# Optimization experiments

Hardware: AMD Instinct MI355X
Metric: run time of the kernel (lower is better)

The kernel has to match this reference:

```python
import jax, jax.numpy as jnp
import numpy as np

N_NODES = 25000
N_EDGES = 400000
D_FEAT = 64      # 2 * per-endpoint feature dim (concat of both endpoints)
STATE_DIM = 16
OUT_DIM = 16
MAX_IT = 5
THRESHOLD = 0.01


def setup_inputs() -> dict:
    key = jax.random.key(0)
    ks = jax.random.split(key, 8)
    edge_src = jax.random.randint(ks[0], (N_EDGES,), 0, N_NODES)
    edge_dst = jax.random.randint(ks[1], (N_EDGES,), 0, N_NODES)
    edge_feat = jax.random.normal(ks[2], (N_EDGES, D_FEAT), jnp.float32)
    w = lambda k, s: jax.random.normal(k, s, jnp.float32) * 0.1
    return {
        "edge_feat": edge_feat,
        "Wst1": w(ks[3], (D_FEAT + STATE_DIM, 2 * STATE_DIM)),
        "bst1": jnp.zeros((2 * STATE_DIM,), jnp.float32),
        "Wst2": w(ks[4], (2 * STATE_DIM, STATE_DIM)),
        "bst2": jnp.zeros((STATE_DIM,), jnp.float32),
        "Wout1": w(ks[5], (STATE_DIM, 2 * STATE_DIM)),
        "bout1": jnp.zeros((2 * STATE_DIM,), jnp.float32),
        "Wout2": w(ks[6], (2 * STATE_DIM, OUT_DIM)),
        "bout2": jnp.zeros((OUT_DIM,), jnp.float32),
        "edge_src": edge_src,
        "edge_dst": edge_dst,
        "n_nodes": N_NODES,
    }


def reference(edge_feat, Wst1, bst1, Wst2, bst2, Wout1, bout1, Wout2, bout2,
              edge_src, edge_dst, n_nodes):
    s = Wst2.shape[1]
    state0 = jnp.zeros((n_nodes, s), edge_feat.dtype)

    def step(carry, _):
        state, done = carry
        gat = state[edge_dst]                                   # [E, s] gather
        x = jnp.concatenate([edge_feat, gat], axis=1)           # [E, 2d+s]
        res = jnp.tanh(jnp.tanh(x @ Wst1 + bst1) @ Wst2 + bst2)  # state MLP
        new_state = jax.ops.segment_sum(res, edge_src, num_segments=n_nodes)
        # per-node L2 change; stop (freeze) once all nodes are below threshold
        dist = jnp.sqrt(jnp.sum((new_state - state) ** 2, axis=1) + 1e-10)
        converged = jnp.all(dist <= THRESHOLD)
        state = jnp.where(done, state, new_state)
        return (state, done | converged), None

    (state, _), _ = jax.lax.scan(step, (state0, jnp.array(False)), None, length=MAX_IT)
    h = jnp.tanh(state @ Wout1 + bout1)
    out = jax.nn.softmax(h @ Wout2 + bout2, axis=-1)  # [n_nodes, out_dim]
    return out
```

## Files before the change

### kernel.cpp

```cpp
#include <hip/hip_runtime.h>
#include <cstddef>

#define D_FEAT 64
#define S_DIM 16
#define H_DIM 32
#define OUT_DIM 16
#define MAX_IT 5

typedef _Float16 half8 __attribute__((ext_vector_type(8)));

__device__ __forceinline__ float fast_tanh(float x) {
    float xc = fminf(fmaxf(x, -15.0f), 15.0f);
    float e = __expf(2.0f * xc);
    return (e - 1.0f) / (e + 1.0f);
}

__global__ __launch_bounds__(256)
void k_hist(const int* __restrict__ src, int* __restrict__ deg, int E) {
    int e = blockIdx.x * 256 + threadIdx.x;
    if (e < E) atomicAdd(&deg[src[e]], 1);
}

__global__ __launch_bounds__(1024)
void k_scan(const int* __restrict__ deg, int* __restrict__ cursor, int N) {
    __shared__ int wsum[16];
    __shared__ int carry;
    int lane = threadIdx.x & 63;
    int wid = threadIdx.x >> 6;
    if (threadIdx.x == 0) carry = 0;
    __syncthreads();
    for (int base = 0; base < N; base += 1024) {
        int i = base + (int)threadIdx.x;
        int v = (i < N) ? deg[i] : 0;
        int incl = v;
#pragma unroll
        for (int off = 1; off < 64; off <<= 1) {
            int t = __shfl_up(incl, off, 64);
            if (lane >= off) incl += t;
        }
        if (lane == 63) wsum[wid] = incl;
        __syncthreads();
        if (wid == 0) {
            int w = (lane < 16) ? wsum[lane] : 0;
            int wi = w;
#pragma unroll
            for (int off = 1; off < 16; off <<= 1) {
                int t = __shfl_up(wi, off, 64);
                if (lane >= off) wi += t;
            }
            if (lane < 16) wsum[lane] = wi - w;
        }
        __syncthreads();
        int excl = incl - v + wsum[wid] + carry;
        if (i < N) cursor[i] = excl;
        __syncthreads();
        if ((int)threadIdx.x == 1023) carry = excl + v;
        __syncthreads();
    }
}

__global__ __launch_bounds__(256)
void k_scatter(const int* __restrict__ src, const int* __restrict__ dst,
               int* __restrict__ cursor, int* __restrict__ pos,
               int* __restrict__ dstp, int* __restrict__ srcp, int E) {
    int e = blockIdx.x * 256 + threadIdx.x;
    if (e >= E) return;
    int s = src[e];
    int p = atomicAdd(&cursor[s], 1);
    pos[e] = p;
    dstp[p] = dst[e];
    srcp[p] = s;
}

__global__ __launch_bounds__(256)
void k_pre(const float* __restrict__ feat, const float* __restrict__ Wst1,
           const float* __restrict__ bst1, const int* __restrict__ pos,
           _Float16* __restrict__ pre, int E) {
    int e = blockIdx.x * 256 + threadIdx.x;
    if (e >= E) return;
    const float4* f4 = reinterpret_cast<const float4*>(feat + (size_t)e * D_FEAT);
    float4 f[16];
#pragma unroll
    for (int k4 = 0; k4 < 16; ++k4) f[k4] = f4[k4];
    int p = pos[e];

    float acc[H_DIM];
#pragma unroll
    for (int j = 0; j < H_DIM; ++j) acc[j] = bst1[j];
#pragma unroll
    for (int k4 = 0; k4 < 16; ++k4) {
        float4 v = f[k4];
        const float* w = Wst1 + k4 * 4 * H_DIM;
#pragma unroll
        for (int j = 0; j < H_DIM; ++j) acc[j] = fmaf(v.x, w[j], acc[j]);
#pragma unroll
        for (int j = 0; j < H_DIM; ++j) acc[j] = fmaf(v.y, w[H_DIM + j], acc[j]);
#pragma unroll
        for (int j = 0; j < H_DIM; ++j) acc[j] = fmaf(v.z, w[2 * H_DIM + j], acc[j]);
#pragma unroll
        for (int j = 0; j < H_DIM; ++j) acc[j] = fmaf(v.w, w[3 * H_DIM + j], acc[j]);
    }
    half8* op = reinterpret_cast<half8*>(pre + (size_t)p * H_DIM);
#pragma unroll
    for (int j8 = 0; j8 < 4; ++j8) {
        half8 v;
#pragma unroll
        for (int k = 0; k < 8; ++k) v[k] = (_Float16)acc[j8 * 8 + k];
        op[j8] = v;
    }
}

__global__ __launch_bounds__(256)
void k_edge(const _Float16* __restrict__ pre, const _Float16* __restrict__ nodeH16,
            const int* __restrict__ dstp, const int* __restrict__ srcp,
            const int* __restrict__ rowend, const float* __restrict__ Wst2,
            const float* __restrict__ bst2, float* __restrict__ new_state,
            const int* __restrict__ flags, int it, int E) {
#pragma unroll
    for (int j = 0; j < MAX_IT; ++j)
        if (j < it && flags[2 + j] == 0) return;
    __shared__ float sres[256][17];
    __shared__ int ssrc[256];
    __shared__ int segnode[256];
    __shared__ int segstart[256];
    __shared__ int segend[256];
    __shared__ int segflag[256];
    __shared__ int nseg;
    const int t = threadIdx.x;
    const int base = blockIdx.x * 256;
    const int ep = base + t;
    const bool valid = ep < E;
    if (t == 0) nseg = 0;

    int s = valid ? srcp[ep] : (int)0x80000000;
    ssrc[t] = s;

    if (valid) {
        half8 n0, n1, n2, n3;
        const bool useH = (it != 0);
        if (useH) {
            int d = dstp[ep];
            const half8* np = reinterpret_cast<const half8*>(nodeH16 + (size_t)d * H_DIM);
            n0 = np[0]; n1 = np[1]; n2 = np[2]; n3 = np[3];
        }
        const half8* pp = reinterpret_cast<const half8*>(pre + (size_t)ep * H_DIM);
        half8 p0 = pp[0], p1 = pp[1], p2 = pp[2], p3 = pp[3];
        float h[H_DIM];
        if (useH) {
#pragma unroll
            for (int k = 0; k < 8; ++k) {
                h[k]      = fast_tanh((float)p0[k] + (float)n0[k]);
                h[8 + k]  = fast_tanh((float)p1[k] + (float)n1[k]);
                h[16 + k] = fast_tanh((float)p2[k] + (float)n2[k]);
                h[24 + k] = fast_tanh((float)p3[k] + (float)n3[k]);
            }
        } else {
#pragma unroll
            for (int k = 0; k < 8; ++k) {
                h[k]      = fast_tanh((float)p0[k]);
                h[8 + k]  = fast_tanh((float)p1[k]);
                h[16 + k] = fast_tanh((float)p2[k]);
                h[24 + k] = fast_tanh((float)p3[k]);
            }
        }
        float r[S_DIM];
#pragma unroll
        for (int i = 0; i < S_DIM; ++i) r[i] = bst2[i];
#pragma unroll
        for (int j = 0; j < H_DIM; ++j) {
            const float* w = Wst2 + (size_t)j * S_DIM;
            float hj = h[j];
#pragma unroll
            for (int i = 0; i < S_DIM; ++i) r[i] = fmaf(hj, w[i], r[i]);
        }
#pragma unroll
        for (int i = 0; i < S_DIM; ++i) sres[t][i] = fast_tanh(r[i]);
    }
    __syncthreads();

    bool head = valid && ((t == 0) || (ssrc[t - 1] != s));
    if (head) {
        int slot = atomicAdd(&nseg, 1);
        int re = rowend[s];
        int en = re - base; if (en > 256) en = 256;
        bool tS = (t > 0) || (ep == 0) || (srcp[ep - 1] != s);
        bool tE = (re <= base + 256);
        segnode[slot] = s;
        segstart[slot] = t;
        segend[slot] = en;
        segflag[slot] = (tS && tE) ? 1 : 0;
    }
    __syncthreads();

    int ns = nseg;
    for (int w = t; w < ns * 16; w += 256) {
        int slot = w >> 4;
        int dim = w & 15;
        int st = segstart[slot];
        int en = segend[slot];
        int node = segnode[slot];
        float a = 0.f;
        for (int i = st; i < en; ++i) a += sres[i][dim];
        float* p = new_state + (size_t)node * S_DIM + dim;
        if (segflag[slot]) *p = a;
        else atomicAdd(p, a);
    }
}

__global__ __launch_bounds__(256)
void k_node(float* __restrict__ state, float* __restrict__ new_state,
            _Float16* __restrict__ nodeH16, const float* __restrict__ Wst1,
            int* __restrict__ flags, int it, int N) {
#pragma unroll
    for (int j = 0; j < MAX_IT; ++j)
        if (j < it && flags[2 + j] == 0) return;
    int tt = blockIdx.x * 256 + threadIdx.x;
    int n = tt >> 2;
    int q = tt & 3;
    if (n >= N) return;
    float4* nsp = reinterpret_cast<float4*>(new_state + (size_t)n * S_DIM);
    float4* sp = reinterpret_cast<float4*>(state + (size_t)n * S_DIM);
    float4 acc = nsp[q];
    float4 old = sp[q];
    float dx = acc.x - old.x, dy = acc.y - old.y, dz = acc.z - old.z, dw = acc.w - old.w;
    float d2 = dx * dx + dy * dy + dz * dz + dw * dw;
    sp[q] = acc;
    nsp[q] = make_float4(0.f, 0.f, 0.f, 0.f);
    d2 += __shfl_xor(d2, 1);
    d2 += __shfl_xor(d2, 2);
    if (q == 0 && d2 + 1e-10f > 1e-4f) flags[2 + it] = 1;

    float st[S_DIM];
    st[q * 4 + 0] = acc.x; st[q * 4 + 1] = acc.y; st[q * 4 + 2] = acc.z; st[q * 4 + 3] = acc.w;
#pragma unroll
    for (int m = 1; m < 4; ++m) {
        int qs = q ^ m;
        st[qs * 4 + 0] = __shfl_xor(acc.x, m);
        st[qs * 4 + 1] = __shfl_xor(acc.y, m);
        st[qs * 4 + 2] = __shfl_xor(acc.z, m);
        st[qs * 4 + 3] = __shfl_xor(acc.w, m);
    }
    float hh[8];
#pragma unroll
    for (int j = 0; j < 8; ++j) hh[j] = 0.f;
#pragma unroll
    for (int k = 0; k < S_DIM; ++k) {
        const float* w = Wst1 + (size_t)(D_FEAT + k) * H_DIM + q * 8;
        float sk = st[k];
#pragma unroll
        for (int j = 0; j < 8; ++j) hh[j] = fmaf(sk, w[j], hh[j]);
    }
    half8 hv;
#pragma unroll
    for (int j = 0; j < 8; ++j) hv[j] = (_Float16)hh[j];
    *reinterpret_cast<half8*>(nodeH16 + (size_t)n * H_DIM + q * 8) = hv;
}

__global__ __launch_bounds__(256)
void gnn_out(const float* __restrict__ state, const float* __restrict__ Wout1,
             const float* __restrict__ bout1, const float* __restrict__ Wout2,
             const float* __restrict__ bout2, float* __restrict__ out, int N) {
    int n = blockIdx.x * 256 + threadIdx.x;
    if (n >= N) return;
    float st[S_DIM];
    const float4* sp = reinterpret_cast<const float4*>(state + (size_t)n * S_DIM);
    float4 v0 = sp[0], v1 = sp[1], v2 = sp[2], v3 = sp[3];
    st[0] = v0.x; st[1] = v0.y; st[2] = v0.z; st[3] = v0.w;
    st[4] = v1.x; st[5] = v1.y; st[6] = v1.z; st[7] = v1.w;
    st[8] = v2.x; st[9] = v2.y; st[10] = v2.z; st[11] = v2.w;
    st[12] = v3.x; st[13] = v3.y; st[14] = v3.z; st[15] = v3.w;

    float h[H_DIM];
#pragma unroll
    for (int j = 0; j < H_DIM; ++j) {
        float acc = bout1[j];
#pragma unroll
        for (int k = 0; k < S_DIM; ++k) acc = fmaf(st[k], Wout1[(size_t)k * H_DIM + j], acc);
        h[j] = fast_tanh(acc);
    }
    float l[OUT_DIM];
#pragma unroll
    for (int i = 0; i < OUT_DIM; ++i) l[i] = bout2[i];
#pragma unroll
    for (int j = 0; j < H_DIM; ++j) {
        float hj = h[j];
#pragma unroll
        for (int i = 0; i < OUT_DIM; ++i) l[i] = fmaf(hj, Wout2[(size_t)j * OUT_DIM + i], l[i]);
    }
    float m = l[0];
#pragma unroll
    for (int i = 1; i < OUT_DIM; ++i) m = fmaxf(m, l[i]);
    float sum = 0.0f;
#pragma unroll
    for (int i = 0; i < OUT_DIM; ++i) {
        float tv = __expf(l[i] - m);
        l[i] = tv;
        sum += tv;
    }
    float inv = 1.0f / sum;
    float4* op = reinterpret_cast<float4*>(out + (size_t)n * OUT_DIM);
    op[0] = make_float4(l[0] * inv, l[1] * inv, l[2] * inv, l[3] * inv);
    op[1] = make_float4(l[4] * inv, l[5] * inv, l[6] * inv, l[7] * inv);
    op[2] = make_float4(l[8] * inv, l[9] * inv, l[10] * inv, l[11] * inv);
    op[3] = make_float4(l[12] * inv, l[13] * inv, l[14] * inv, l[15] * inv);
}

extern "C" void kernel_launch(void* const* d_in, const int* in_sizes, int n_in,
                              void* d_out, int out_size, void* d_ws, size_t ws_size,
                              hipStream_t stream) {
    const float* edge_feat = (const float*)d_in[0];
    const float* Wst1 = (const float*)d_in[1];
    const float* bst1 = (const float*)d_in[2];
    const float* Wst2 = (const float*)d_in[3];
    const float* bst2 = (const float*)d_in[4];
    const float* Wout1 = (const float*)d_in[5];
    const float* bout1 = (const float*)d_in[6];
    const float* Wout2 = (const float*)d_in[7];
    const float* bout2 = (const float*)d_in[8];
    const int* esrc = (const int*)d_in[9];
    const int* edst = (const int*)d_in[10];
    const int E = in_sizes[9];
    const int N = out_size / OUT_DIM;
    float* out = (float*)d_out;

    float* state = (float*)d_ws;
    float* new_state = state + (size_t)N * S_DIM;
    _Float16* pre = (_Float16*)(new_state + (size_t)N * S_DIM);
    _Float16* nodeH16 = pre + (size_t)E * H_DIM;
    int* pos = (int*)(nodeH16 + (size_t)N * H_DIM);
    int* dstp = pos + E;
    int* srcp = dstp + E;
    int* deg = srcp + E;
    int* cursor = deg + N;
    int* flags = cursor + N;

    hipMemsetAsync(state, 0, (size_t)N * S_DIM * 2 * sizeof(float), stream);
    hipMemsetAsync(deg, 0, (size_t)N * sizeof(int), stream);
    hipMemsetAsync(flags, 0, 8 * sizeof(int), stream);

    int ebl = (E + 255) / 256;
    int nbl = (N + 255) / 256;
    int rbl = (N * 4 + 255) / 256;

    k_hist<<<ebl, 256, 0, stream>>>(esrc, deg, E);
    k_scan<<<1, 1024, 0, stream>>>(deg, cursor, N);
    k_scatter<<<ebl, 256, 0, stream>>>(esrc, edst, cursor, pos, dstp, srcp, E);
    k_pre<<<ebl, 256, 0, stream>>>(edge_feat, Wst1, bst1, pos, pre, E);

    for (int it = 0; it < MAX_IT; ++it) {
        k_edge<<<ebl, 256, 0, stream>>>(pre, nodeH16, dstp, srcp, cursor, Wst2, bst2,
                                        new_state, flags, it, E);
        k_node<<<rbl, 256, 0, stream>>>(state, new_state, nodeH16, Wst1, flags, it, N);
    }
    gnn_out<<<nbl, 256, 0, stream>>>(state, Wout1, bout1, Wout2, bout2, out, N);
}
```

Baseline: 290.1 us.

## Use split-fp16 MFMA for edge pre-projection and single-pass node scan

The per-edge feat@Wst1 projection moves from scalar FMA loops to MFMA 16x16x32 fp16 instructions. Both the features and the weights are split into hi and lo fp16 parts, with three MFMAs per tile to keep close to fp32 accuracy. Results are staged through shared memory so each lane can write contiguous 8-half chunks to the permuted output positions. The degree exclusive scan also changes from a serial multi-pass block loop to a per-thread chunk scan with a single block-level combine. The scan rewrite trades coalesced reads for strided per-thread loops, and the MFMA path adds a __syncthreads per tile.

```diff
diff --git a/kernel.cpp b/kernel.cpp
--- a/kernel.cpp
+++ b/kernel.cpp
@@ -8,6 +8,8 @@
 #define MAX_IT 5
 
 typedef _Float16 half8 __attribute__((ext_vector_type(8)));
+typedef _Float16 f16x8 __attribute__((ext_vector_type(8)));
+typedef float f32x4 __attribute__((ext_vector_type(4)));
 
 __device__ __forceinline__ float fast_tanh(float x) {
     float xc = fminf(fmaxf(x, -15.0f), 15.0f);
@@ -24,38 +26,37 @@
 __global__ __launch_bounds__(1024)
 void k_scan(const int* __restrict__ deg, int* __restrict__ cursor, int N) {
     __shared__ int wsum[16];
-    __shared__ int carry;
-    int lane = threadIdx.x & 63;
-    int wid = threadIdx.x >> 6;
-    if (threadIdx.x == 0) carry = 0;
+    const int t = threadIdx.x;
+    const int lane = t & 63;
+    const int wid = t >> 6;
+    const int chunk = (N + 1023) / 1024;
+    const int start = t * chunk;
+    const int end = min(start + chunk, N);
+    int sum = 0;
+    for (int i = start; i < end; ++i) sum += deg[i];
+    int incl = sum;
+#pragma unroll
+    for (int off = 1; off < 64; off <<= 1) {
+        int u = __shfl_up(incl, off, 64);
+        if (lane >= off) incl += u;
+    }
+    if (lane == 63) wsum[wid] = incl;
     __syncthreads();
-    for (int base = 0; base < N; base += 1024) {
-        int i = base + (int)threadIdx.x;
-        int v = (i < N) ? deg[i] : 0;
-        int incl = v;
-#pragma unroll
-        for (int off = 1; off < 64; off <<= 1) {
-            int t = __shfl_up(incl, off, 64);
-            if (lane >= off) incl += t;
-        }
-        if (lane == 63) wsum[wid] = incl;
-        __syncthreads();
-        if (wid == 0) {
-            int w = (lane < 16) ? wsum[lane] : 0;
-            int wi = w;
-#pragma unroll
-            for (int off = 1; off < 16; off <<= 1) {
-                int t = __shfl_up(wi, off, 64);
-                if (lane >= off) wi += t;
-            }
-            if (lane < 16) wsum[lane] = wi - w;
-        }
-        __syncthreads();
-        int excl = incl - v + wsum[wid] + carry;
-        if (i < N) cursor[i] = excl;
-        __syncthreads();
-        if ((int)threadIdx.x == 1023) carry = excl + v;
-        __syncthreads();
+    if (wid == 0) {
+        int w = (lane < 16) ? wsum[lane] : 0;
+        int wi = w;
+#pragma unroll
+        for (int off = 1; off < 16; off <<= 1) {
+            int u = __shfl_up(wi, off, 64);
+            if (lane >= off) wi += u;
+        }
+        if (lane < 16) wsum[lane] = wi - w;
+    }
+    __syncthreads();
+    int run = incl - sum + wsum[wid];
+    for (int i = start; i < end; ++i) {
+        cursor[i] = run;
+        run += deg[i];
     }
 }
 
@@ -76,37 +77,79 @@
 void k_pre(const float* __restrict__ feat, const float* __restrict__ Wst1,
            const float* __restrict__ bst1, const int* __restrict__ pos,
            _Float16* __restrict__ pre, int E) {
-    int e = blockIdx.x * 256 + threadIdx.x;
-    if (e >= E) return;
-    const float4* f4 = reinterpret_cast<const float4*>(feat + (size_t)e * D_FEAT);
-    float4 f[16];
-#pragma unroll
-    for (int k4 = 0; k4 < 16; ++k4) f[k4] = f4[k4];
-    int p = pos[e];
-
-    float acc[H_DIM];
-#pragma unroll
-    for (int j = 0; j < H_DIM; ++j) acc[j] = bst1[j];
-#pragma unroll
-    for (int k4 = 0; k4 < 16; ++k4) {
-        float4 v = f[k4];
-        const float* w = Wst1 + k4 * 4 * H_DIM;
-#pragma unroll
-        for (int j = 0; j < H_DIM; ++j) acc[j] = fmaf(v.x, w[j], acc[j]);
-#pragma unroll
-        for (int j = 0; j < H_DIM; ++j) acc[j] = fmaf(v.y, w[H_DIM + j], acc[j]);
-#pragma unroll
-        for (int j = 0; j < H_DIM; ++j) acc[j] = fmaf(v.z, w[2 * H_DIM + j], acc[j]);
-#pragma unroll
-        for (int j = 0; j < H_DIM; ++j) acc[j] = fmaf(v.w, w[3 * H_DIM + j], acc[j]);
-    }
-    half8* op = reinterpret_cast<half8*>(pre + (size_t)p * H_DIM);
-#pragma unroll
-    for (int j8 = 0; j8 < 4; ++j8) {
-        half8 v;
-#pragma unroll
-        for (int k = 0; k < 8; ++k) v[k] = (_Float16)acc[j8 * 8 + k];
-        op[j8] = v;
+    __shared__ _Float16 sD[2][4][16][40];
+    const int t = threadIdx.x;
+    const int wave = t >> 6;
+    const int lane = t & 63;
+    const int col = lane & 15;
+    const int kg = lane >> 4;
+    const int wbase = blockIdx.x * 256 + wave * 64;
+
+    f16x8 Bh[2][2], Bl[2][2];
+#pragma unroll
+    for (int kt = 0; kt < 2; ++kt)
+#pragma unroll
+        for (int nt = 0; nt < 2; ++nt)
+#pragma unroll
+            for (int i = 0; i < 8; ++i) {
+                float wv = Wst1[(size_t)(kt * 32 + kg * 8 + i) * H_DIM + nt * 16 + col];
+                _Float16 hi = (_Float16)wv;
+                Bh[kt][nt][i] = hi;
+                Bl[kt][nt][i] = (_Float16)(wv - (float)hi);
+            }
+    float bias0 = bst1[col];
+    float bias1 = bst1[16 + col];
+
+#pragma unroll
+    for (int mt = 0; mt < 4; ++mt) {
+        const int row = wbase + mt * 16 + col;
+        const bool rv = row < E;
+        f16x8 Ah[2], Al[2];
+#pragma unroll
+        for (int kt = 0; kt < 2; ++kt) {
+            float av[8];
+            if (rv) {
+                const float4* fp = reinterpret_cast<const float4*>(
+                    feat + (size_t)row * D_FEAT + kt * 32 + kg * 8);
+                float4 a0 = fp[0], a1 = fp[1];
+                av[0] = a0.x; av[1] = a0.y; av[2] = a0.z; av[3] = a0.w;
+                av[4] = a1.x; av[5] = a1.y; av[6] = a1.z; av[7] = a1.w;
+            } else {
+#pragma unroll
+                for (int i = 0; i < 8; ++i) av[i] = 0.f;
+            }
+#pragma unroll
+            for (int i = 0; i < 8; ++i) {
+                _Float16 hi = (_Float16)av[i];
+                Ah[kt][i] = hi;
+                Al[kt][i] = (_Float16)(av[i] - (float)hi);
+            }
+        }
+        f32x4 acc0 = {0.f, 0.f, 0.f, 0.f};
+        f32x4 acc1 = {0.f, 0.f, 0.f, 0.f};
+#pragma unroll
+        for (int kt = 0; kt < 2; ++kt) {
+            acc0 = __builtin_amdgcn_mfma_f32_16x16x32_f16(Ah[kt], Bh[kt][0], acc0, 0, 0, 0);
+            acc0 = __builtin_amdgcn_mfma_f32_16x16x32_f16(Al[kt], Bh[kt][0], acc0, 0, 0, 0);
+            acc0 = __builtin_amdgcn_mfma_f32_16x16x32_f16(Ah[kt], Bl[kt][0], acc0, 0, 0, 0);
+            acc1 = __builtin_amdgcn_mfma_f32_16x16x32_f16(Ah[kt], Bh[kt][1], acc1, 0, 0, 0);
+            acc1 = __builtin_amdgcn_mfma_f32_16x16x32_f16(Al[kt], Bh[kt][1], acc1, 0, 0, 0);
+            acc1 = __builtin_amdgcn_mfma_f32_16x16x32_f16(Ah[kt], Bl[kt][1], acc1, 0, 0, 0);
+        }
+        const int par = mt & 1;
+#pragma unroll
+        for (int r = 0; r < 4; ++r) {
+            sD[par][wave][kg * 4 + r][col] = (_Float16)(acc0[r] + bias0);
+            sD[par][wave][kg * 4 + r][16 + col] = (_Float16)(acc1[r] + bias1);
+        }
+        __syncthreads();
+        if (rv) {
+            int p = pos[row];
+            f16x8 v;
+#pragma unroll
+            for (int i = 0; i < 8; ++i) v[i] = sD[par][wave][col][kg * 8 + i];
+            *reinterpret_cast<f16x8*>(pre + (size_t)p * H_DIM + kg * 8) = v;
+        }
     }
 }
 
```

Result: faster. 282.2 us (-2.7%).
